# Performance work log

Hardware: AMD Instinct MI355X
Metric: run time of the kernel (lower is better)

Reference implementation:

```python
import jax, jax.numpy as jnp
import numpy as np

TEMPERATURE = 0.07
EPS = 1e-8  # torch F.cosine_similarity default eps on the norm product


def setup_inputs() -> dict:
    key = jax.random.key(0)
    k1, k2 = jax.random.split(key)
    emb1 = jax.random.normal(k1, (8192, 128), dtype=jnp.float32)
    emb2 = jax.random.normal(k2, (8192, 128), dtype=jnp.float32)
    return {"emb1": emb1, "emb2": emb2}


def reference(emb1, emb2):
    B1 = emb1.shape[0]
    n1 = jnp.linalg.norm(emb1, axis=1)  # [B1]
    n2 = jnp.linalg.norm(emb2, axis=1)  # [B2]

    # Pairwise cosine similarities via GEMM + clamped norm product (matches F.cosine_similarity eps).
    sim11 = (emb1 @ emb1.T) / jnp.maximum(n1[:, None] * n1[None, :], EPS)  # [B1,B1]
    sim12 = (emb1 @ emb2.T) / jnp.maximum(n1[:, None] * n2[None, :], EPS)  # [B1,B2]

    # loss1 replicates the original loop: for i, for j in [i+1, B1): pair (i, (i+j) % B1).
    I = jnp.arange(B1)[:, None]
    J = jnp.arange(B1)[None, :]
    K = (I + J) % B1                                   # gathered column index
    mask = J > I                                       # j in [i+1, B1)
    vals = jnp.take_along_axis(sim11, K, axis=1)       # sim11[i, (i+j)%B1]
    loss1 = jnp.sum(jnp.where(mask, jnp.exp(vals / TEMPERATURE), 0.0))

    # loss2: all cross pairs between emb1 and emb2.
    loss2 = jnp.sum(jnp.exp(sim12 / TEMPERATURE))

    return (-jnp.log(loss1 / loss2)).reshape(1)
```

## Files before the change

kernel.cpp:

```cpp
#include <hip/hip_runtime.h>

#define B_ROWS   8192
#define BMASK    8191
#define DIM      128
#define CTILE    64
#define CHUNK    8
#define BLK64    16384

typedef __attribute__((ext_vector_type(8)))  __bf16 bf16x8;
typedef __attribute__((ext_vector_type(16))) float  f32x16;

#define RBSCALE 4.5398159f

__device__ __forceinline__ float fast_exp2(float x) {
    return exp2f(x);
}

__global__ __launch_bounds__(256)
void prep_kernel(const float* __restrict__ e1, const float* __restrict__ e2,
                 char* __restrict__ p1, char* __restrict__ p2,
                 float* __restrict__ acc) {
    if (blockIdx.x == 0 && threadIdx.x < 4) acc[threadIdx.x] = 0.f;
    const int rb = blockIdx.x;
    const float* src; char* dst; int rb_loc;
    if (rb < 128) { src = e1; dst = p1; rb_loc = rb; }
    else          { src = e2; dst = p2; rb_loc = rb - 128; }

    const int t  = threadIdx.x;
    const int rr = t >> 2;
    const int q  = t & 3;

    const float* rp = src + (size_t)(rb_loc * 64 + rr) * DIM + q * 32;
    float4 f[8];
    float ss = 0.f;
#pragma unroll
    for (int j = 0; j < 8; ++j) {
        f[j] = ((const float4*)rp)[j];
        ss += f[j].x * f[j].x + f[j].y * f[j].y + f[j].z * f[j].z + f[j].w * f[j].w;
    }
    ss += __shfl_xor(ss, 1);
    ss += __shfl_xor(ss, 2);
    const float rbn = RBSCALE / sqrtf(ss);

    char* db = dst + (size_t)rb_loc * BLK64;
#pragma unroll
    for (int j = 0; j < 4; ++j) {
        bf16x8 v;
        float4 a = f[2 * j], b = f[2 * j + 1];
        v[0] = (__bf16)(a.x * rbn); v[1] = (__bf16)(a.y * rbn);
        v[2] = (__bf16)(a.z * rbn); v[3] = (__bf16)(a.w * rbn);
        v[4] = (__bf16)(b.x * rbn); v[5] = (__bf16)(b.y * rbn);
        v[6] = (__bf16)(b.z * rbn); v[7] = (__bf16)(b.w * rbn);
        *(bf16x8*)(db + (size_t)(q * 4 + j) * 1024 + (size_t)rr * 16) = v;
    }
}

template <bool MASKED>
__device__ __forceinline__ float tile_sum(const f32x16& a0, const f32x16& a1,
                                          int i00, int c) {
    float s = 0.f;
#pragma unroll
    for (int g = 0; g < 2; ++g) {
        const f32x16& a = g ? a1 : a0;
        int ib = i00 + g * 32;
#pragma unroll
        for (int r = 0; r < 16; ++r) {
            float ev = fast_exp2(a[r]);
            if (MASKED) {
                int i = ib + (r & 3) + 8 * (r >> 2);
                int d = (c - i) & BMASK;
                s += (d > i) ? ev : 0.f;
            } else {
                s += ev;
            }
        }
    }
    return s;
}

__global__ __launch_bounds__(256, 4)
void pair_kernel(const char* __restrict__ P1, const char* __restrict__ P2,
                 float* __restrict__ accg, float* __restrict__ out,
                 int nz0, int nblocks) {
    __shared__ __align__(16) __bf16 Bbuf[2][8192];
    __shared__ float red[4];

    const int tid = threadIdx.x;
    const int b   = blockIdx.x;

    int z, p, k0, k1;
    if (b < nz0) {
        z = 0;
        int accb = 0; p = 0;
        for (;; ++p) {
            int i0t = 128 * p;
            int e1t = (i0t > 128) ? i0t : 128;
            int cnt = 2 + (B_ROWS - e1t) / 64;
            int nb  = (cnt + CHUNK - 1) / CHUNK;
            if (b < accb + nb) {
                int s = b - accb;
                k0 = s * CHUNK;
                k1 = (k0 + CHUNK < cnt) ? (k0 + CHUNK) : cnt;
                break;
            }
            accb += nb;
        }
    } else {
        z = 1;
        int j = b - nz0;
        p  = j >> 4;
        k0 = (j & 15) * CHUNK;
        k1 = k0 + CHUNK;
    }
    const int i0 = 128 * p;
    const int e1 = (i0 > 128) ? i0 : 128;

    const char* Bpack = (z == 0) ? P1 : P2;

    auto tile_c0 = [&](int k) -> int {
        if (z) return k * CTILE;
        int e = (k == 0) ? 64 : e1 + (k - 1) * 64;
        return (i0 + e) & BMASK;
    };
    auto tile_masked = [&](int k) -> bool {
        if (z) return false;
        int e = (k == 0) ? 64 : e1 + (k - 1) * 64;
        return (e < i0 + 256) || (e > 8128);
    };

    const int w  = tid >> 6, lane = tid & 63;
    const int w2 = w >> 1, wc = w & 1;
    const int l  = lane & 31, h = lane >> 5;

    bf16x8 af[2][8];
    {
        const char* ap = P1 + (size_t)(p * 2 + w2) * BLK64;
#pragma unroll
        for (int g = 0; g < 2; ++g)
#pragma unroll
            for (int s = 0; s < 8; ++s)
                af[g][s] = *(const bf16x8*)(ap + (size_t)(s * 2 + h) * 1024
                                               + (size_t)(g * 32 + l) * 16);
    }

    auto stage = [&](int bufi, int k) {
        const char* gp = Bpack + (size_t)(tile_c0(k) >> 6) * BLK64 + (size_t)tid * 16;
        char*       lp = (char*)&Bbuf[bufi][0] + (size_t)tid * 16;
#pragma unroll
        for (int r = 0; r < 4; ++r)
            __builtin_amdgcn_global_load_lds(
                (const __attribute__((address_space(1))) unsigned int*)(gp + r * 4096),
                (__attribute__((address_space(3))) unsigned int*)(lp + r * 4096),
                16, 0, 0);
    };

    const int i00 = i0 + w2 * 64 + 4 * h;
    const int cb  = wc * 32 + l;

    float sacc = 0.f;
    stage(0, k0);
    int cur = 0;
    for (int k = k0; k < k1; ++k) {
        __syncthreads();
        if (k + 1 < k1) stage(cur ^ 1, k + 1);

        f32x16 a0, a1;
#pragma unroll
        for (int r = 0; r < 16; ++r) { a0[r] = 0.f; a1[r] = 0.f; }

        const char* bb = (const char*)&Bbuf[cur][0] + (size_t)cb * 16 + (size_t)h * 1024;
#pragma unroll
        for (int s = 0; s < 8; ++s) {
            bf16x8 bf = *(const bf16x8*)(bb + (size_t)s * 2048);
            a0 = __builtin_amdgcn_mfma_f32_32x32x16_bf16(af[0][s], bf, a0, 0, 0, 0);
            a1 = __builtin_amdgcn_mfma_f32_32x32x16_bf16(af[1][s], bf, a1, 0, 0, 0);
        }

        int c = tile_c0(k) + cb;
        sacc += tile_masked(k) ? tile_sum<true >(a0, a1, i00, c)
                               : tile_sum<false>(a0, a1, i00, c);
        cur ^= 1;
    }

#pragma unroll
    for (int o = 32; o > 0; o >>= 1) sacc += __shfl_down(sacc, o);
    if (lane == 0) red[w] = sacc;
    __syncthreads();
    if (tid == 0) {
        atomicAdd(&accg[z], red[0] + red[1] + red[2] + red[3]);
        __threadfence();
        unsigned prev = atomicAdd((unsigned*)&accg[2], 1u);
        if (prev == (unsigned)(nblocks - 1)) {
            float l1 = atomicAdd(&accg[0], 0.f);
            float l2 = atomicAdd(&accg[1], 0.f);
            out[0] = -logf(l1 / l2);
        }
    }
}

extern "C" void kernel_launch(void* const* d_in, const int* in_sizes, int n_in,
                              void* d_out, int out_size, void* d_ws, size_t ws_size,
                              hipStream_t stream) {
    (void)in_sizes; (void)n_in; (void)out_size; (void)ws_size;
    const float* e1 = (const float*)d_in[0];
    const float* e2 = (const float*)d_in[1];
    float* out = (float*)d_out;
    char*  ws  = (char*)d_ws;

    float* acc = (float*)ws;
    char*  p1  = ws + 4096;
    char*  p2  = ws + 4096 + 2097152;

    int nz0 = 0;
    for (int p = 0; p < 64; ++p) {
        int i0 = 128 * p;
        int e1t = (i0 > 128) ? i0 : 128;
        int cnt = 2 + (B_ROWS - e1t) / 64;
        nz0 += (cnt + CHUNK - 1) / CHUNK;
    }
    int nblocks = nz0 + 1024;

    prep_kernel<<<dim3(256), dim3(256), 0, stream>>>(e1, e2, p1, p2, acc);
    pair_kernel<<<dim3(nblocks), dim3(256), 0, stream>>>(p1, p2, acc, out, nz0, nblocks);
}
```

Before: 124.6 us.

## Merge self and cross tile work into fixed 1024 balanced blocks

Replaces the separate z=0 (sim11 triangular) and z=1 (sim12) block ranges with a fixed 1024-block grid. Each block handles up to 8 self-similarity tiles plus 8 cross tiles for its row panel, keeping two accumulators. Blocks with few triangular tiles get cross-tile work alongside, which is meant to balance load and remove the host-side block-count computation and the per-block search loop. Occupancy hint drops from 4 to 3 waves-per-EU, which may change register allocation.

```diff
diff --git a/kernel.cpp b/kernel.cpp
--- a/kernel.cpp
+++ b/kernel.cpp
@@ -3,18 +3,13 @@
 #define B_ROWS   8192
 #define BMASK    8191
 #define DIM      128
-#define CTILE    64
-#define CHUNK    8
 #define BLK64    16384
+#define NBLOCKS  1024
 
 typedef __attribute__((ext_vector_type(8)))  __bf16 bf16x8;
 typedef __attribute__((ext_vector_type(16))) float  f32x16;
 
 #define RBSCALE 4.5398159f
-
-__device__ __forceinline__ float fast_exp2(float x) {
-    return exp2f(x);
-}
 
 __global__ __launch_bounds__(256)
 void prep_kernel(const float* __restrict__ e1, const float* __restrict__ e2,
@@ -65,7 +60,7 @@
         int ib = i00 + g * 32;
 #pragma unroll
         for (int r = 0; r < 16; ++r) {
-            float ev = fast_exp2(a[r]);
+            float ev = exp2f(a[r]);
             if (MASKED) {
                 int i = ib + (r & 3) + 8 * (r >> 2);
                 int d = (c - i) & BMASK;
@@ -78,53 +73,38 @@
     return s;
 }
 
-__global__ __launch_bounds__(256, 4)
+__global__ __launch_bounds__(256, 3)
 void pair_kernel(const char* __restrict__ P1, const char* __restrict__ P2,
-                 float* __restrict__ accg, float* __restrict__ out,
-                 int nz0, int nblocks) {
+                 float* __restrict__ accg, float* __restrict__ out) {
     __shared__ __align__(16) __bf16 Bbuf[2][8192];
-    __shared__ float red[4];
+    __shared__ float red[2][4];
 
     const int tid = threadIdx.x;
     const int b   = blockIdx.x;
-
-    int z, p, k0, k1;
-    if (b < nz0) {
-        z = 0;
-        int accb = 0; p = 0;
-        for (;; ++p) {
-            int i0t = 128 * p;
-            int e1t = (i0t > 128) ? i0t : 128;
-            int cnt = 2 + (B_ROWS - e1t) / 64;
-            int nb  = (cnt + CHUNK - 1) / CHUNK;
-            if (b < accb + nb) {
-                int s = b - accb;
-                k0 = s * CHUNK;
-                k1 = (k0 + CHUNK < cnt) ? (k0 + CHUNK) : cnt;
-                break;
-            }
-            accb += nb;
-        }
-    } else {
-        z = 1;
-        int j = b - nz0;
-        p  = j >> 4;
-        k0 = (j & 15) * CHUNK;
-        k1 = k0 + CHUNK;
-    }
-    const int i0 = 128 * p;
-    const int e1 = (i0 > 128) ? i0 : 128;
-
-    const char* Bpack = (z == 0) ? P1 : P2;
-
-    auto tile_c0 = [&](int k) -> int {
-        if (z) return k * CTILE;
-        int e = (k == 0) ? 64 : e1 + (k - 1) * 64;
-        return (i0 + e) & BMASK;
+    const int p   = b & 63;
+    const int s   = b >> 6;
+
+    const int i0  = 128 * p;
+    const int e1  = (i0 > 128) ? i0 : 128;
+    const int cnt = (p < 2) ? 128 : (130 - 2 * p);
+
+    int n0 = cnt - 8 * s;
+    n0 = (n0 < 0) ? 0 : ((n0 > 8) ? 8 : n0);
+    const int L = n0 + 8;
+
+    auto tile_src = [&](int m) -> const char* { return (m < n0) ? P1 : P2; };
+    auto tile_c0  = [&](int m) -> int {
+        if (m < n0) {
+            int k = 8 * s + m;
+            int e = (k == 0) ? 64 : e1 + 64 * (k - 1);
+            return (i0 + e) & BMASK;
+        }
+        return 64 * (8 * s + (m - n0));
     };
-    auto tile_masked = [&](int k) -> bool {
-        if (z) return false;
-        int e = (k == 0) ? 64 : e1 + (k - 1) * 64;
+    auto tile_masked = [&](int m) -> bool {
+        if (m >= n0) return false;
+        int k = 8 * s + m;
+        int e = (k == 0) ? 64 : e1 + 64 * (k - 1);
         return (e < i0 + 256) || (e > 8128);
     };
 
@@ -138,13 +118,13 @@
 #pragma unroll
         for (int g = 0; g < 2; ++g)
 #pragma unroll
-            for (int s = 0; s < 8; ++s)
-                af[g][s] = *(const bf16x8*)(ap + (size_t)(s * 2 + h) * 1024
-                                               + (size_t)(g * 32 + l) * 16);
-    }
-
-    auto stage = [&](int bufi, int k) {
-        const char* gp = Bpack + (size_t)(tile_c0(k) >> 6) * BLK64 + (size_t)tid * 16;
+            for (int sc = 0; sc < 8; ++sc)
+                af[g][sc] = *(const bf16x8*)(ap + (size_t)(sc * 2 + h) * 1024
+                                                + (size_t)(g * 32 + l) * 16);
+    }
+
+    auto stage = [&](int bufi, int m) {
+        const char* gp = tile_src(m) + (size_t)(tile_c0(m) >> 6) * BLK64 + (size_t)tid * 16;
         char*       lp = (char*)&Bbuf[bufi][0] + (size_t)tid * 16;
 #pragma unroll
         for (int r = 0; r < 4; ++r)
@@ -157,12 +137,12 @@
     const int i00 = i0 + w2 * 64 + 4 * h;
     const int cb  = wc * 32 + l;
 
-    float sacc = 0.f;
-    stage(0, k0);
+    float s0 = 0.f, s1 = 0.f;
+    stage(0, 0);
     int cur = 0;
-    for (int k = k0; k < k1; ++k) {
+    for (int m = 0; m < L; ++m) {
         __syncthreads();
-        if (k + 1 < k1) stage(cur ^ 1, k + 1);
+        if (m + 1 < L) stage(cur ^ 1, m + 1);
 
         f32x16 a0, a1;
 #pragma unroll
@@ -170,27 +150,32 @@
 
         const char* bb = (const char*)&Bbuf[cur][0] + (size_t)cb * 16 + (size_t)h * 1024;
 #pragma unroll
-        for (int s = 0; s < 8; ++s) {
-            bf16x8 bf = *(const bf16x8*)(bb + (size_t)s * 2048);
-            a0 = __builtin_amdgcn_mfma_f32_32x32x16_bf16(af[0][s], bf, a0, 0, 0, 0);
-            a1 = __builtin_amdgcn_mfma_f32_32x32x16_bf16(af[1][s], bf, a1, 0, 0, 0);
-        }
-
-        int c = tile_c0(k) + cb;
-        sacc += tile_masked(k) ? tile_sum<true >(a0, a1, i00, c)
-                               : tile_sum<false>(a0, a1, i00, c);
+        for (int sc = 0; sc < 8; ++sc) {
+            bf16x8 bf = *(const bf16x8*)(bb + (size_t)sc * 2048);
+            a0 = __builtin_amdgcn_mfma_f32_32x32x16_bf16(af[0][sc], bf, a0, 0, 0, 0);
+            a1 = __builtin_amdgcn_mfma_f32_32x32x16_bf16(af[1][sc], bf, a1, 0, 0, 0);
+        }
+
+        int c = tile_c0(m) + cb;
+        float ts = tile_masked(m) ? tile_sum<true >(a0, a1, i00, c)
+                                  : tile_sum<false>(a0, a1, i00, c);
+        if (m < n0) s0 += ts; else s1 += ts;
         cur ^= 1;
     }
 
 #pragma unroll
-    for (int o = 32; o > 0; o >>= 1) sacc += __shfl_down(sacc, o);
-    if (lane == 0) red[w] = sacc;
+    for (int o = 32; o > 0; o >>= 1) {
+        s0 += __shfl_down(s0, o);
+        s1 += __shfl_down(s1, o);
+    }
+    if (lane == 0) { red[0][w] = s0; red[1][w] = s1; }
     __syncthreads();
     if (tid == 0) {
-        atomicAdd(&accg[z], red[0] + red[1] + red[2] + red[3]);
+        atomicAdd(&accg[0], red[0][0] + red[0][1] + red[0][2] + red[0][3]);
+        atomicAdd(&accg[1], red[1][0] + red[1][1] + red[1][2] + red[1][3]);
         __threadfence();
         unsigned prev = atomicAdd((unsigned*)&accg[2], 1u);
-        if (prev == (unsigned)(nblocks - 1)) {
+        if (prev == (unsigned)(NBLOCKS - 1)) {
             float l1 = atomicAdd(&accg[0], 0.f);
             float l2 = atomicAdd(&accg[1], 0.f);
             out[0] = -logf(l1 / l2);
@@ -211,15 +196,6 @@
     char*  p1  = ws + 4096;
     char*  p2  = ws + 4096 + 2097152;
 
-    int nz0 = 0;
-    for (int p = 0; p < 64; ++p) {
-        int i0 = 128 * p;
-        int e1t = (i0 > 128) ? i0 : 128;
-        int cnt = 2 + (B_ROWS - e1t) / 64;
-        nz0 += (cnt + CHUNK - 1) / CHUNK;
-    }
-    int nblocks = nz0 + 1024;
-
     prep_kernel<<<dim3(256), dim3(256), 0, stream>>>(e1, e2, p1, p2, acc);
-    pair_kernel<<<dim3(nblocks), dim3(256), 0, stream>>>(p1, p2, acc, out, nz0, nblocks);
-}
+    pair_kernel<<<dim3(NBLOCKS), dim3(256), 0, stream>>>(p1, p2, acc, out);
+}
```

New measurement: 129.4 us. 3.8% more time.
